# Performance work log

Measured on AMD Instinct MI355X. Metric: run time of the kernel, lower is better.

Reference implementation:

```python
import jax, jax.numpy as jnp
import numpy as np
from jax import lax

L, H, C, V, BLK = 6, 12, 768, 50257, 1024
B, T = 4, 1024
HD = C // H
EPS = 1e-5


def _norm(key, shape, scale=0.02):
    return jax.random.normal(key, shape, dtype=jnp.float32) * scale


def setup_inputs() -> dict:
    key = jax.random.key(0)
    ks = jax.random.split(key, 16)
    idx = jax.random.randint(ks[0], (B, T), 0, V)
    inp = {
        "idx": idx,
        "wte": _norm(ks[1], (V, C)),
        "wpe": _norm(ks[2], (BLK, C)),
        "ln1_s": jnp.ones((L, C)),
        "ln1_b": jnp.zeros((L, C)),
        "qkv_w": _norm(ks[3], (L, C, 3 * C)),
        "qkv_b": jnp.zeros((L, 3 * C)),
        "proj_w": _norm(ks[4], (L, C, C)),
        "proj_b": jnp.zeros((L, C)),
        "ln2_s": jnp.ones((L, C)),
        "ln2_b": jnp.zeros((L, C)),
        "fc_w": _norm(ks[5], (L, C, 4 * C)),
        "fc_b": jnp.zeros((L, 4 * C)),
        "fcp_w": _norm(ks[6], (L, 4 * C, C)),
        "fcp_b": jnp.zeros((L, C)),
        "lnf_s": jnp.ones((C,)),
        "lnf_b": jnp.zeros((C,)),
    }
    return inp


def layer_norm(x, s, b):
    mu = jnp.mean(x, axis=-1, keepdims=True)
    var = jnp.mean(jnp.square(x - mu), axis=-1, keepdims=True)
    return (x - mu) * lax.rsqrt(var + EPS) * s + b


def block(x, p):
    ln1_s, ln1_b, qkv_w, qkv_b, proj_w, proj_b, ln2_s, ln2_b, fc_w, fc_b, fcp_w, fcp_b = p
    Bx, Tx, Cx = x.shape
    h = layer_norm(x, ln1_s, ln1_b)
    qkv = h @ qkv_w + qkv_b  # [B,T,3C]
    q, k, v = jnp.split(qkv, 3, axis=-1)
    q = q.reshape(Bx, Tx, H, HD).swapaxes(1, 2)  # [B,H,T,hd]
    k = k.reshape(Bx, Tx, H, HD).swapaxes(1, 2)
    v = v.reshape(Bx, Tx, H, HD).swapaxes(1, 2)
    attn = jnp.einsum("bhqd,bhkd->bhqk", q, k) / jnp.sqrt(jnp.float32(HD))
    mask = jnp.tril(jnp.ones((Tx, Tx), dtype=bool))
    attn = jnp.where(mask, attn, -jnp.inf)
    attn = jax.nn.softmax(attn, axis=-1)
    y = jnp.einsum("bhqk,bhkd->bhqd", attn, v)
    y = y.swapaxes(1, 2).reshape(Bx, Tx, Cx)
    x = x + (y @ proj_w + proj_b)
    h = layer_norm(x, ln2_s, ln2_b)
    h = jax.nn.gelu(h @ fc_w + fc_b, approximate=True)
    x = x + (h @ fcp_w + fcp_b)
    return x


def reference(idx, wte, wpe, ln1_s, ln1_b, qkv_w, qkv_b, proj_w, proj_b,
              ln2_s, ln2_b, fc_w, fc_b, fcp_w, fcp_b, lnf_s, lnf_b):
    Tx = idx.shape[1]
    x = wte[idx] + wpe[:Tx][None]  # [B,T,C]
    params = (ln1_s, ln1_b, qkv_w, qkv_b, proj_w, proj_b,
              ln2_s, ln2_b, fc_w, fc_b, fcp_w, fcp_b)
    def step(carry, p):
        return block(carry, p), None
    x, _ = lax.scan(step, x, params)
    x = layer_norm(x, lnf_s, lnf_b)
    logits = x @ wte.T  # tied embedding attend
    return logits
```

## Files before the change

kernel.cpp:

```cpp
#include <hip/hip_runtime.h>
#include <math.h>

#define LNUM 6
#define HNUM 12
#define CDIM 768
#define VDIM 50257
#define BDIM 4
#define TDIM 1024
#define NTOK 4096

typedef __bf16 bf16;
typedef __bf16 bf16x8 __attribute__((ext_vector_type(8)));
typedef float  floatx4 __attribute__((ext_vector_type(4)));
typedef unsigned int u32;

__device__ inline void gload16(const bf16* gsrc, bf16* lds) {
  __builtin_amdgcn_global_load_lds(
      (const __attribute__((address_space(1))) u32*)gsrc,
      (__attribute__((address_space(3))) u32*)lds, 16, 0, 0);
}

__global__ void k_cvt_bf16(const float* __restrict__ in, bf16* __restrict__ out, long n) {
  long i = ((long)blockIdx.x * blockDim.x + threadIdx.x) * 4;
  long stride = (long)gridDim.x * blockDim.x * 4;
  for (; i < n; i += stride) {
    float4 v = *reinterpret_cast<const float4*>(in + i);
    bf16 b0 = (bf16)v.x, b1 = (bf16)v.y, b2 = (bf16)v.z, b3 = (bf16)v.w;
    ushort4 pk;
    pk.x = __builtin_bit_cast(unsigned short, b0);
    pk.y = __builtin_bit_cast(unsigned short, b1);
    pk.z = __builtin_bit_cast(unsigned short, b2);
    pk.w = __builtin_bit_cast(unsigned short, b3);
    *reinterpret_cast<ushort4*>(out + i) = pk;
  }
}

#define TILES_QKV  1728
#define TILES_PROJ 576
#define TILES_FC   2304
#define TILES_FCP  2304
#define TILES_LAYER (TILES_QKV + TILES_PROJ + TILES_FC + TILES_FCP)

__global__ __launch_bounds__(256) void k_trans_all(
    const float* __restrict__ qkv_w, const float* __restrict__ proj_w,
    const float* __restrict__ fc_w, const float* __restrict__ fcp_w,
    bf16* __restrict__ wq, bf16* __restrict__ wp,
    bf16* __restrict__ wf, bf16* __restrict__ wfp) {
  __shared__ float tile[32][33];
  int bid = blockIdx.x;
  int layer = bid / TILES_LAYER, r = bid % TILES_LAYER;
  const float* src; bf16* dst; int K, N, tx, ty;
  if (r < TILES_QKV) {
    src = qkv_w + (size_t)layer * CDIM * 3 * CDIM; dst = wq + (size_t)layer * CDIM * 3 * CDIM;
    K = CDIM; N = 3 * CDIM; tx = r % 72; ty = r / 72;
  } else if (r < TILES_QKV + TILES_PROJ) {
    r -= TILES_QKV;
    src = proj_w + (size_t)layer * CDIM * CDIM; dst = wp + (size_t)layer * CDIM * CDIM;
    K = CDIM; N = CDIM; tx = r % 24; ty = r / 24;
  } else if (r < TILES_QKV + TILES_PROJ + TILES_FC) {
    r -= TILES_QKV + TILES_PROJ;
    src = fc_w + (size_t)layer * CDIM * 4 * CDIM; dst = wf + (size_t)layer * CDIM * 4 * CDIM;
    K = CDIM; N = 4 * CDIM; tx = r % 96; ty = r / 96;
  } else {
    r -= TILES_QKV + TILES_PROJ + TILES_FC;
    src = fcp_w + (size_t)layer * 4 * CDIM * CDIM; dst = wfp + (size_t)layer * 4 * CDIM * CDIM;
    K = 4 * CDIM; N = CDIM; tx = r % 24; ty = r / 24;
  }
  int n0 = tx * 32, k0 = ty * 32;
  int nx = threadIdx.x & 31, tyy = threadIdx.x >> 5;
  #pragma unroll
  for (int p = 0; p < 4; ++p) {
    int k = tyy + p * 8;
    tile[k][nx] = src[(size_t)(k0 + k) * N + n0 + nx];
  }
  __syncthreads();
  #pragma unroll
  for (int p = 0; p < 4; ++p) {
    int n = tyy + p * 8;
    dst[(size_t)(n0 + n) * K + k0 + nx] = (bf16)tile[nx][n];
  }
}

__global__ void k_embed(const int* __restrict__ idx, const float* __restrict__ wte,
                        const float* __restrict__ wpe, float* __restrict__ x) {
  int tok = blockIdx.x;
  int t = tok & (TDIM - 1);
  int id = idx[tok];
  const float* a = wte + (size_t)id * CDIM;
  const float* p = wpe + (size_t)t * CDIM;
  float* o = x + (size_t)tok * CDIM;
  for (int c = threadIdx.x; c < CDIM; c += 256) o[c] = a[c] + p[c];
}

__global__ __launch_bounds__(256) void k_layernorm(const float* __restrict__ x,
    const float* __restrict__ sc, const float* __restrict__ bi, bf16* __restrict__ out) {
  __shared__ float red[8];
  int row = blockIdx.x;
  const float* xr = x + (size_t)row * CDIM;
  int t = threadIdx.x;
  float v0 = xr[t], v1 = xr[t + 256], v2 = xr[t + 512];
  float s = v0 + v1 + v2;
  #pragma unroll
  for (int o = 32; o > 0; o >>= 1) s += __shfl_down(s, o);
  if ((t & 63) == 0) red[t >> 6] = s;
  __syncthreads();
  float mean = (red[0] + red[1] + red[2] + red[3]) * (1.0f / CDIM);
  float d0 = v0 - mean, d1 = v1 - mean, d2 = v2 - mean;
  float q = d0 * d0 + d1 * d1 + d2 * d2;
  #pragma unroll
  for (int o = 32; o > 0; o >>= 1) q += __shfl_down(q, o);
  if ((t & 63) == 0) red[4 + (t >> 6)] = q;
  __syncthreads();
  float var = (red[4] + red[5] + red[6] + red[7]) * (1.0f / CDIM);
  float rs = rsqrtf(var + 1e-5f);
  bf16* orow = out + (size_t)row * CDIM;
  orow[t]       = (bf16)(d0 * rs * sc[t]       + bi[t]);
  orow[t + 256] = (bf16)(d1 * rs * sc[t + 256] + bi[t + 256]);
  orow[t + 512] = (bf16)(d2 * rs * sc[t + 512] + bi[t + 512]);
}

__device__ inline float gelu_f(float x) {
  float x3 = x * x * x;
  return 0.5f * x * (1.0f + tanhf(0.7978845608028654f * (x + 0.044715f * x3)));
}

template<int EPI>
__global__ __launch_bounds__(512, 1) void k_gemm8(
    const bf16* __restrict__ A, const bf16* __restrict__ Bt,
    const float* __restrict__ bias,
    float* __restrict__ Cf, bf16* __restrict__ Cb,
    int N, int K) {
  __shared__ __align__(16) bf16 lds[2][4][8192];
  const int nwg = gridDim.x;
  const int id = blockIdx.x;
  const int swz = (id & 7) * (nwg >> 3) + (id >> 3);
  const int m0 = (swz & 15) * 256;
  const int n0 = (swz >> 4) * 256;
  const int tid = threadIdx.x, lane = tid & 63, wave = tid >> 6;
  const int wr = wave >> 2, wc = wave & 3;
  const int g = lane >> 4, r16 = lane & 15;
  const int numK = K >> 6;
  const int wsl = wave * 512;

  const int srow = wave * 16 + (lane >> 2);
  const int scol = ((lane & 3) ^ ((lane >> 3) & 3)) * 8;
  const bf16* at  = A  + (size_t)(m0 + srow) * K + scol;
  const bf16* at1 = A  + (size_t)(m0 + srow + 128) * K + scol;
  const bf16* bt  = Bt + (size_t)(n0 + srow) * K + scol;
  const bf16* bt1 = Bt + (size_t)(n0 + srow + 128) * K + scol;
  const int sw = (g ^ ((r16 >> 1) & 3)) * 8;
  const int a_off = (wr * 128 + r16) * 32 + sw;
  const int b_off = (wc * 64 + r16) * 32 + sw;

  floatx4 acc[8][4] = {};

#define G2(sA, sB, dst) do { gload16((sA), (dst)); gload16((sB), (dst) + 4096); } while (0)

  G2(bt,      bt1,      &lds[0][0][wsl]);
  G2(at,      at1,      &lds[0][1][wsl]);
  G2(bt + 32, bt1 + 32, &lds[0][2][wsl]);
  G2(at + 32, at1 + 32, &lds[0][3][wsl]);
  G2(bt + 64, bt1 + 64, &lds[1][0][wsl]);
  G2(at + 64, at1 + 64, &lds[1][1][wsl]);
  G2(bt + 96, bt1 + 96, &lds[1][2][wsl]);
  asm volatile("s_waitcnt vmcnt(6)" ::: "memory");
  __builtin_amdgcn_s_barrier();

  for (int t = 0; t < numK; ++t) {
    const int p = t & 1, pn = p ^ 1;
    bf16x8 af[4], bfr[4];

    #pragma unroll
    for (int j = 0; j < 4; ++j) bfr[j] = *(const bf16x8*)&lds[p][0][b_off + j * 512];
    #pragma unroll
    for (int i = 0; i < 4; ++i) af[i] = *(const bf16x8*)&lds[p][1][a_off + i * 512];
    if (t + 1 < numK) G2(at + 96, at1 + 96, &lds[pn][3][wsl]);
    __builtin_amdgcn_s_barrier();
    asm volatile("s_waitcnt lgkmcnt(0)" ::: "memory");
    __builtin_amdgcn_s_setprio(1);
    #pragma unroll
    for (int i = 0; i < 4; ++i)
      #pragma unroll
      for (int j = 0; j < 4; ++j)
        acc[i][j] = __builtin_amdgcn_mfma_f32_16x16x32_bf16(af[i], bfr[j], acc[i][j], 0, 0, 0);
    __builtin_amdgcn_s_setprio(0);
    __builtin_amdgcn_s_barrier();

    #pragma unroll
    for (int i = 0; i < 4; ++i) af[i] = *(const bf16x8*)&lds[p][1][a_off + (i + 4) * 512];
    if (t + 2 < numK) G2(bt + 128, bt1 + 128, &lds[p][0][wsl]);
    __builtin_amdgcn_s_barrier();
    asm volatile("s_waitcnt lgkmcnt(0)" ::: "memory");
    __builtin_amdgcn_s_setprio(1);
    #pragma unroll
    for (int i = 0; i < 4; ++i)
      #pragma unroll
      for (int j = 0; j < 4; ++j)
        acc[i + 4][j] = __builtin_amdgcn_mfma_f32_16x16x32_bf16(af[i], bfr[j], acc[i + 4][j], 0, 0, 0);
    __builtin_amdgcn_s_setprio(0);
    __builtin_amdgcn_s_barrier();

    #pragma unroll
    for (int j = 0; j < 4; ++j) bfr[j] = *(const bf16x8*)&lds[p][2][b_off + j * 512];
    #pragma unroll
    for (int i = 0; i < 4; ++i) af[i] = *(const bf16x8*)&lds[p][3][a_off + i * 512];
    if (t + 2 < numK) G2(at + 128, at1 + 128, &lds[p][1][wsl]);
    __builtin_amdgcn_s_barrier();
    asm volatile("s_waitcnt lgkmcnt(0)" ::: "memory");
    __builtin_amdgcn_s_setprio(1);
    #pragma unroll
    for (int i = 0; i < 4; ++i)
      #pragma unroll
      for (int j = 0; j < 4; ++j)
        acc[i][j] = __builtin_amdgcn_mfma_f32_16x16x32_bf16(af[i], bfr[j], acc[i][j], 0, 0, 0);
    __builtin_amdgcn_s_setprio(0);
    __builtin_amdgcn_s_barrier();

    #pragma unroll
    for (int i = 0; i < 4; ++i) af[i] = *(const bf16x8*)&lds[p][3][a_off + (i + 4) * 512];
    if (t + 2 < numK) G2(bt + 160, bt1 + 160, &lds[p][2][wsl]);
    __builtin_amdgcn_s_barrier();
    asm volatile("s_waitcnt lgkmcnt(0)" ::: "memory");
    __builtin_amdgcn_s_setprio(1);
    #pragma unroll
    for (int i = 0; i < 4; ++i)
      #pragma unroll
      for (int j = 0; j < 4; ++j)
        acc[i + 4][j] = __builtin_amdgcn_mfma_f32_16x16x32_bf16(af[i], bfr[j], acc[i + 4][j], 0, 0, 0);
    __builtin_amdgcn_s_setprio(0);
    if (t + 2 < numK) { asm volatile("s_waitcnt vmcnt(6)" ::: "memory"); }
    else              { asm volatile("s_waitcnt vmcnt(0)" ::: "memory"); }
    __builtin_amdgcn_s_barrier();

    at += 64; at1 += 64; bt += 64; bt1 += 64;
  }
#undef G2

  if (EPI == 0) {
    float* sb = reinterpret_cast<float*>(&lds[0][0][0]) + wave * 1088;
    const int seg = lane & 15, rq = lane >> 4;
    const int mrow_base = m0 + wr * 128;
    const int ncol_base = n0 + wc * 64;
    #pragma unroll
    for (int mf = 0; mf < 8; ++mf) {
      #pragma unroll
      for (int nf = 0; nf < 4; ++nf) {
        #pragma unroll
        for (int q = 0; q < 4; ++q)
          sb[(g * 4 + q) * 68 + nf * 16 + r16] = acc[mf][nf][q];
      }
      #pragma unroll
      for (int pz = 0; pz < 4; ++pz) {
        int row = rq + pz * 4;
        floatx4 v = *reinterpret_cast<const floatx4*>(&sb[row * 68 + seg * 4]);
        int m = mrow_base + mf * 16 + row;
        int n = ncol_base + seg * 4;
        if (n + 4 <= N) {
          __builtin_memcpy(&Cf[(size_t)m * N + n], &v, 16);
        } else {
          #pragma unroll
          for (int e = 0; e < 4; ++e)
            if (n + e < N) Cf[(size_t)m * N + n + e] = v[e];
        }
      }
    }
  } else {
    bf16* sb = &lds[0][0][0] + wave * 1152;
    const int rr_rd = lane & 15, seg = lane >> 4;
    const int nb = n0 + wc * 64 + r16;
    float bv[4];
    #pragma unroll
    for (int j = 0; j < 4; ++j) bv[j] = bias[nb + j * 16];
    #pragma unroll
    for (int mf = 0; mf < 8; ++mf) {
      #pragma unroll
      for (int j = 0; j < 4; ++j) {
        #pragma unroll
        for (int q = 0; q < 4; ++q) {
          float v = acc[mf][j][q] + bv[j];
          if (EPI == 3) v = gelu_f(v);
          sb[(g * 4 + q) * 72 + j * 16 + r16] = (bf16)v;
        }
      }
      bf16x8 o0 = *(const bf16x8*)&sb[rr_rd * 72 + seg * 16];
      bf16x8 o1 = *(const bf16x8*)&sb[rr_rd * 72 + seg * 16 + 8];
      size_t orow = (size_t)(m0 + wr * 128 + mf * 16 + rr_rd) * N + (n0 + wc * 64 + seg * 16);
      *(bf16x8*)&Cb[orow] = o0;
      *(bf16x8*)&Cb[orow + 8] = o1;
    }
  }
}

template<int TBM, int MI, int NI, int EPI>
__global__ __launch_bounds__(256) void k_gemm(
    const bf16* __restrict__ A, const bf16* __restrict__ Bt,
    const float* __restrict__ bias, const float* __restrict__ resid,
    float* __restrict__ Cf, bf16* __restrict__ Cb,
    int M, int N, int K) {
  constexpr int BN = 128;
  constexpr int WGN = BN / (NI * 16);
  constexpr int AI = TBM / 32;
  constexpr int BI = BN / 32;
  __shared__ __align__(16) bf16 As[TBM * 64];
  __shared__ __align__(16) bf16 Bs[BN * 64];
  const int m0 = blockIdx.x * TBM, n0 = blockIdx.y * BN;
  const int tid = threadIdx.x;
  const int lane = tid & 63, wave = tid >> 6;
  const int wr = wave / WGN, wc = wave % WGN;
  const int l8 = lane >> 3, s8 = lane & 7;
  const int g = lane >> 4, r16 = lane & 15;

  floatx4 acc[MI][NI] = {};

  const bf16* a_src = A + (size_t)(m0 + l8) * K + s8 * 8;
  const bf16* b_src = Bt + (size_t)(n0 + l8) * K + s8 * 8;

  for (int k0 = 0; k0 < K; k0 += 64) {
    #pragma unroll
    for (int t = 0; t < AI; ++t) {
      int row0 = wave * (TBM / 4) + t * 8;
      gload16(a_src + (size_t)row0 * K + k0, &As[row0 * 64]);
    }
    #pragma unroll
    for (int t = 0; t < BI; ++t) {
      int row0 = wave * 32 + t * 8;
      gload16(b_src + (size_t)row0 * K + k0, &Bs[row0 * 64]);
    }
    __syncthreads();
    #pragma unroll
    for (int kk = 0; kk < 2; ++kk) {
      bf16x8 af[MI], bfr[NI];
      #pragma unroll
      for (int i = 0; i < MI; ++i)
        af[i] = *reinterpret_cast<const bf16x8*>(&As[(wr * MI * 16 + i * 16 + r16) * 64 + g * 8 + kk * 32]);
      #pragma unroll
      for (int j = 0; j < NI; ++j)
        bfr[j] = *reinterpret_cast<const bf16x8*>(&Bs[(wc * NI * 16 + j * 16 + r16) * 64 + g * 8 + kk * 32]);
      #pragma unroll
      for (int i = 0; i < MI; ++i) {
        #pragma unroll
        for (int j = 0; j < NI; ++j)
          acc[i][j] = __builtin_amdgcn_mfma_f32_16x16x32_bf16(af[i], bfr[j], acc[i][j], 0, 0, 0);
      }
    }
    __syncthreads();
  }

  int mb = m0 + wr * MI * 16 + g * 4;
  int nb = n0 + wc * NI * 16 + r16;
  #pragma unroll
  for (int j = 0; j < NI; ++j) {
    int n = nb + j * 16;
    if (n >= N) continue;
    float bv = (EPI >= 2) ? bias[n] : 0.0f;
    #pragma unroll
    for (int i = 0; i < MI; ++i) {
      #pragma unroll
      for (int q = 0; q < 4; ++q) {
        int m = mb + i * 16 + q;
        float v = acc[i][j][q] + bv;
        size_t o = (size_t)m * N + n;
        if (EPI == 2)      Cf[o] = v + resid[o];
        else if (EPI == 3) Cb[o] = (bf16)gelu_f(v);
        else if (EPI == 4) Cb[o] = (bf16)v;
        else               Cf[o] = v;
      }
    }
  }
}

__global__ __launch_bounds__(256) void k_vtrans(const bf16* __restrict__ qkv, bf16* __restrict__ vt) {
  __shared__ bf16 tile[64][72];
  int bh = blockIdx.x, t0 = blockIdx.y * 64;
  int b = bh / HNUM, h = bh % HNUM;
  int tid = threadIdx.x;
  int r8 = tid >> 3, s8 = tid & 7;
  #pragma unroll
  for (int p = 0; p < 2; ++p) {
    int row = p * 32 + r8;
    uint4 v = *reinterpret_cast<const uint4*>(
        qkv + (size_t)(b * TDIM + t0 + row) * (3 * CDIM) + 2 * CDIM + h * 64 + s8 * 8);
    *reinterpret_cast<uint4*>(&tile[row][s8 * 8]) = v;
  }
  __syncthreads();
  int d = tid >> 2, q4 = tid & 3;
  #pragma unroll
  for (int half = 0; half < 2; ++half) {
    int t = q4 * 16 + half * 8;
    bf16x8 o;
    #pragma unroll
    for (int u = 0; u < 8; ++u) o[u] = tile[t + u][d];
    *reinterpret_cast<bf16x8*>(vt + (size_t)bh * (64 * TDIM) + (size_t)d * TDIM + t0 + t) = o;
  }
}

__global__ __launch_bounds__(256) void k_attn(const bf16* __restrict__ qkv,
                                              const bf16* __restrict__ vt,
                                              bf16* __restrict__ y) {
  __shared__ __align__(16) bf16 Ks[64 * 64];
  __shared__ __align__(16) bf16 Vs[64 * 64];
  __shared__ __align__(16) bf16 Ps[64 * 64];
  const int bh = blockIdx.x, qt = blockIdx.y;
  const int b = bh / HNUM, h = bh % HNUM;
  const int tid = threadIdx.x, lane = tid & 63, wave = tid >> 6;
  const int g = lane >> 4, r16 = lane & 15;
  const int w16 = wave * 16;
  const int r8 = tid >> 3, s8 = tid & 7;

  bf16x8 qf[2];
  {
    const bf16* qsrc = qkv + (size_t)(b * TDIM + qt * 64 + w16 + r16) * (3 * CDIM) + h * 64 + g * 8;
    qf[0] = *reinterpret_cast<const bf16x8*>(qsrc);
    qf[1] = *reinterpret_cast<const bf16x8*>(qsrc + 32);
  }

  float m_r[4], l_r[4];
  floatx4 yacc[4] = {};
  #pragma unroll
  for (int q = 0; q < 4; ++q) { m_r[q] = -1e30f; l_r[q] = 0.f; }

  for (int kt = 0; kt <= qt; ++kt) {
    __syncthreads();
    #pragma unroll
    for (int p = 0; p < 2; ++p) {
      int row = p * 32 + r8;
      uint4 kv = *reinterpret_cast<const uint4*>(
          qkv + (size_t)(b * TDIM + kt * 64 + row) * (3 * CDIM) + CDIM + h * 64 + s8 * 8);
      *reinterpret_cast<uint4*>(&Ks[row * 64 + ((s8 ^ (row & 7)) * 8)]) = kv;
      uint4 vv = *reinterpret_cast<const uint4*>(
          vt + (size_t)bh * (64 * TDIM) + (size_t)row * TDIM + kt * 64 + s8 * 8);
      *reinterpret_cast<uint4*>(&Vs[row * 64 + ((s8 ^ (row & 7)) * 8)]) = vv;
    }
    __syncthreads();

    floatx4 sa[4] = {};
    #pragma unroll
    for (int c = 0; c < 2; ++c) {
      bf16x8 kf[4];
      #pragma unroll
      for (int j = 0; j < 4; ++j) {
        int krow = j * 16 + r16;
        kf[j] = *reinterpret_cast<const bf16x8*>(&Ks[krow * 64 + (((g + 4 * c) ^ (krow & 7)) * 8)]);
      }
      #pragma unroll
      for (int j = 0; j < 4; ++j)
        sa[j] = __builtin_amdgcn_mfma_f32_16x16x32_bf16(qf[c], kf[j], sa[j], 0, 0, 0);
    }

    const bool diag = (kt == qt);
    float p_v[4][4];
    #pragma unroll
    for (int q = 0; q < 4; ++q) {
      int qrow = w16 + g * 4 + q;
      float mx = -1e30f;
      #pragma unroll
      for (int j = 0; j < 4; ++j) {
        float s = sa[j][q] * 0.125f;
        if (diag && (r16 + j * 16) > qrow) s = -1e30f;
        p_v[j][q] = s;
        mx = fmaxf(mx, s);
      }
      #pragma unroll
      for (int o = 1; o < 16; o <<= 1) mx = fmaxf(mx, __shfl_xor(mx, o));
      float mnew = fmaxf(m_r[q], mx);
      float ps = 0.f;
      #pragma unroll
      for (int j = 0; j < 4; ++j) {
        float p = __expf(p_v[j][q] - mnew);
        p_v[j][q] = p;
        ps += p;
      }
      #pragma unroll
      for (int o = 1; o < 16; o <<= 1) ps += __shfl_xor(ps, o);
      float alpha = __expf(m_r[q] - mnew);
      m_r[q] = mnew;
      l_r[q] = l_r[q] * alpha + ps;
      #pragma unroll
      for (int j = 0; j < 4; ++j) yacc[j][q] *= alpha;
      #pragma unroll
      for (int j = 0; j < 4; ++j) {
        int col = r16 + j * 16;
        Ps[qrow * 64 + (col ^ ((qrow & 7) << 3))] = (bf16)p_v[j][q];
      }
    }

    #pragma unroll
    for (int ks = 0; ks < 2; ++ks) {
      int prow = w16 + r16;
      bf16x8 pa = *reinterpret_cast<const bf16x8*>(&Ps[prow * 64 + (((g + 4 * ks) ^ (prow & 7)) * 8)]);
      #pragma unroll
      for (int j = 0; j < 4; ++j) {
        int vrow = j * 16 + r16;
        bf16x8 vb = *reinterpret_cast<const bf16x8*>(&Vs[vrow * 64 + (((g + 4 * ks) ^ (vrow & 7)) * 8)]);
        yacc[j] = __builtin_amdgcn_mfma_f32_16x16x32_bf16(pa, vb, yacc[j], 0, 0, 0);
      }
    }
  }

  #pragma unroll
  for (int q = 0; q < 4; ++q) {
    float inv = 1.0f / l_r[q];
    int tok = b * TDIM + qt * 64 + w16 + g * 4 + q;
    #pragma unroll
    for (int j = 0; j < 4; ++j)
      y[(size_t)tok * CDIM + h * 64 + r16 + j * 16] = (bf16)(yacc[j][q] * inv);
  }
}

extern "C" void kernel_launch(void* const* d_in, const int* in_sizes, int n_in,
                              void* d_out, int out_size, void* d_ws, size_t ws_size,
                              hipStream_t stream) {
  (void)in_sizes; (void)n_in; (void)out_size;
  const int*   idx    = (const int*)  d_in[0];
  const float* wte    = (const float*)d_in[1];
  const float* wpe    = (const float*)d_in[2];
  const float* ln1_s  = (const float*)d_in[3];
  const float* ln1_b  = (const float*)d_in[4];
  const float* qkv_w  = (const float*)d_in[5];
  const float* qkv_b  = (const float*)d_in[6];
  const float* proj_w = (const float*)d_in[7];
  const float* proj_b = (const float*)d_in[8];
  const float* ln2_s  = (const float*)d_in[9];
  const float* ln2_b  = (const float*)d_in[10];
  const float* fc_w   = (const float*)d_in[11];
  const float* fc_b   = (const float*)d_in[12];
  const float* fcp_w  = (const float*)d_in[13];
  const float* fcp_b  = (const float*)d_in[14];
  const float* lnf_s  = (const float*)d_in[15];
  const float* lnf_b  = (const float*)d_in[16];
  float* logits = (float*)d_out;

  char* base = (char*)d_ws;
  size_t off = 0;
  auto alloc = [&](size_t bytes) -> void* {
    void* p = base + off;
    off += (bytes + 255) & ~(size_t)255;
    return p;
  };
  bf16*  wte_bf  = (bf16*) alloc((size_t)VDIM * CDIM * 2);
  bf16*  wq_all  = (bf16*) alloc((size_t)LNUM * 3 * CDIM * CDIM * 2);
  bf16*  wp_all  = (bf16*) alloc((size_t)LNUM * CDIM * CDIM * 2);
  bf16*  wf_all  = (bf16*) alloc((size_t)LNUM * 4 * CDIM * CDIM * 2);
  bf16*  wfp_all = (bf16*) alloc((size_t)LNUM * 4 * CDIM * CDIM * 2);
  float* x       = (float*)alloc((size_t)NTOK * CDIM * 4);
  bf16*  hb      = (bf16*) alloc((size_t)NTOK * CDIM * 2);
  bf16*  qkv_bf  = (bf16*) alloc((size_t)NTOK * 3 * CDIM * 2);
  bf16*  vt      = (bf16*) alloc((size_t)BDIM * HNUM * 64 * TDIM * 2);
  bf16*  yb      = (bf16*) alloc((size_t)NTOK * CDIM * 2);
  bf16*  gb      = (bf16*) alloc((size_t)NTOK * 4 * CDIM * 2);
  if (off > ws_size) return;

  k_cvt_bf16<<<4096, 256, 0, stream>>>(wte, wte_bf, (long)VDIM * CDIM);
  k_trans_all<<<LNUM * TILES_LAYER, 256, 0, stream>>>(qkv_w, proj_w, fc_w, fcp_w,
                                                      wq_all, wp_all, wf_all, wfp_all);
  k_embed<<<NTOK, 256, 0, stream>>>(idx, wte, wpe, x);

  for (int l = 0; l < LNUM; ++l) {
    const bf16* wq  = wq_all  + (size_t)l * 3 * CDIM * CDIM;
    const bf16* wp  = wp_all  + (size_t)l * CDIM * CDIM;
    const bf16* wf  = wf_all  + (size_t)l * 4 * CDIM * CDIM;
    const bf16* wfp = wfp_all + (size_t)l * 4 * CDIM * CDIM;

    k_layernorm<<<NTOK, 256, 0, stream>>>(x, ln1_s + l*CDIM, ln1_b + l*CDIM, hb);
    k_gemm8<4><<<16 * 9, 512, 0, stream>>>(hb, wq, qkv_b + (size_t)l*3*CDIM, nullptr, qkv_bf, 3*CDIM, CDIM);
    k_vtrans<<<dim3(BDIM*HNUM, TDIM/64), 256, 0, stream>>>(qkv_bf, vt);
    k_attn<<<dim3(BDIM*HNUM, TDIM/64), 256, 0, stream>>>(qkv_bf, vt, yb);
    k_gemm<64,4,2,2><<<dim3(NTOK/64, 6), 256, 0, stream>>>(yb, wp, proj_b + (size_t)l*CDIM, x, x, nullptr, NTOK, CDIM, CDIM);
    k_layernorm<<<NTOK, 256, 0, stream>>>(x, ln2_s + l*CDIM, ln2_b + l*CDIM, hb);
    k_gemm8<3><<<16 * 12, 512, 0, stream>>>(hb, wf, fc_b + (size_t)l*4*CDIM, nullptr, gb, 4*CDIM, CDIM);
    k_gemm<64,4,2,2><<<dim3(NTOK/64, 6), 256, 0, stream>>>(gb, wfp, fcp_b + (size_t)l*CDIM, x, x, nullptr, NTOK, CDIM, 4*CDIM);
  }

  k_layernorm<<<NTOK, 256, 0, stream>>>(x, lnf_s, lnf_b, hb);
  int ntile = (VDIM + 255) / 256;
  k_gemm8<0><<<16 * ntile, 512, 0, stream>>>(hb, wte_bf, nullptr, logits, nullptr, VDIM, CDIM);
}
```

Before: 1.839 ms.

## Template k_gemm8 on M tile size and halve K-step per pipeline iteration

Makes the 8-wave GEMM kernel templated on M tile height (128 or 256) and shrinks each pipeline iteration from K=64 to K=32 with a two-stage LDS buffer. The QKV and FC GEMMs switch to 128-row tiles, doubling workgroup count (288 and 384 blocks) so more CUs are busy on these small-N problems. The logits GEMM keeps 256-row tiles but also uses the new shorter K step. Shared memory per block drops, at the cost of more barriers per unit of work and less reuse per loaded B tile.

```diff
diff --git a/kernel.cpp b/kernel.cpp
--- a/kernel.cpp
+++ b/kernel.cpp
@@ -124,22 +124,27 @@
   return 0.5f * x * (1.0f + tanhf(0.7978845608028654f * (x + 0.044715f * x3)));
 }
 
-template<int EPI>
+template<int TBM, int EPI>
 __global__ __launch_bounds__(512, 1) void k_gemm8(
     const bf16* __restrict__ A, const bf16* __restrict__ Bt,
     const float* __restrict__ bias,
     float* __restrict__ Cf, bf16* __restrict__ Cb,
     int N, int K) {
-  __shared__ __align__(16) bf16 lds[2][4][8192];
+  constexpr int MI = TBM / 32;
+  constexpr int MH = MI / 2;
+  constexpr int MTILES = 4096 / TBM;
+  __shared__ __align__(16) bf16 smem[2 * 8192 + 2 * TBM * 32];
+  bf16* Bs = smem;
+  bf16* As = smem + 2 * 8192;
   const int nwg = gridDim.x;
   const int id = blockIdx.x;
   const int swz = (id & 7) * (nwg >> 3) + (id >> 3);
-  const int m0 = (swz & 15) * 256;
-  const int n0 = (swz >> 4) * 256;
+  const int m0 = (swz % MTILES) * TBM;
+  const int n0 = (swz / MTILES) * 256;
   const int tid = threadIdx.x, lane = tid & 63, wave = tid >> 6;
   const int wr = wave >> 2, wc = wave & 3;
   const int g = lane >> 4, r16 = lane & 15;
-  const int numK = K >> 6;
+  const int numK = K >> 5;
   const int wsl = wave * 512;
 
   const int srow = wave * 16 + (lane >> 2);
@@ -149,37 +154,36 @@
   const bf16* bt  = Bt + (size_t)(n0 + srow) * K + scol;
   const bf16* bt1 = Bt + (size_t)(n0 + srow + 128) * K + scol;
   const int sw = (g ^ ((r16 >> 1) & 3)) * 8;
-  const int a_off = (wr * 128 + r16) * 32 + sw;
+  const int a_off = (wr * (TBM / 2) + r16) * 32 + sw;
   const int b_off = (wc * 64 + r16) * 32 + sw;
 
-  floatx4 acc[8][4] = {};
-
-#define G2(sA, sB, dst) do { gload16((sA), (dst)); gload16((sB), (dst) + 4096); } while (0)
-
-  G2(bt,      bt1,      &lds[0][0][wsl]);
-  G2(at,      at1,      &lds[0][1][wsl]);
-  G2(bt + 32, bt1 + 32, &lds[0][2][wsl]);
-  G2(at + 32, at1 + 32, &lds[0][3][wsl]);
-  G2(bt + 64, bt1 + 64, &lds[1][0][wsl]);
-  G2(at + 64, at1 + 64, &lds[1][1][wsl]);
-  G2(bt + 96, bt1 + 96, &lds[1][2][wsl]);
-  asm volatile("s_waitcnt vmcnt(6)" ::: "memory");
+  floatx4 acc[MI][4] = {};
+
+#define STB(s0, s1, pb) do { gload16((s0), Bs + (pb) * 8192 + wsl); \
+                             gload16((s1), Bs + (pb) * 8192 + wsl + 4096); } while (0)
+#define STA(s0, s1, pb) do { gload16((s0), As + (pb) * TBM * 32 + wsl); \
+                             if constexpr (TBM == 256) gload16((s1), As + (pb) * TBM * 32 + wsl + 4096); } while (0)
+
+  STB(bt, bt1, 0);
+  STA(at, at1, 0);
+  STB(bt + 32, bt1 + 32, 1);
+  asm volatile("s_waitcnt vmcnt(2)" ::: "memory");
   __builtin_amdgcn_s_barrier();
 
   for (int t = 0; t < numK; ++t) {
     const int p = t & 1, pn = p ^ 1;
-    bf16x8 af[4], bfr[4];
-
-    #pragma unroll
-    for (int j = 0; j < 4; ++j) bfr[j] = *(const bf16x8*)&lds[p][0][b_off + j * 512];
-    #pragma unroll
-    for (int i = 0; i < 4; ++i) af[i] = *(const bf16x8*)&lds[p][1][a_off + i * 512];
-    if (t + 1 < numK) G2(at + 96, at1 + 96, &lds[pn][3][wsl]);
+    bf16x8 af[MH], bfr[4];
+
+    #pragma unroll
+    for (int j = 0; j < 4; ++j) bfr[j] = *(const bf16x8*)&Bs[p * 8192 + b_off + j * 512];
+    #pragma unroll
+    for (int i = 0; i < MH; ++i) af[i] = *(const bf16x8*)&As[p * TBM * 32 + a_off + i * 512];
+    if (t + 1 < numK) STA(at + 32, at1 + 32, pn);
     __builtin_amdgcn_s_barrier();
     asm volatile("s_waitcnt lgkmcnt(0)" ::: "memory");
     __builtin_amdgcn_s_setprio(1);
     #pragma unroll
-    for (int i = 0; i < 4; ++i)
+    for (int i = 0; i < MH; ++i)
       #pragma unroll
       for (int j = 0; j < 4; ++j)
         acc[i][j] = __builtin_amdgcn_mfma_f32_16x16x32_bf16(af[i], bfr[j], acc[i][j], 0, 0, 0);
@@ -187,62 +191,33 @@
     __builtin_amdgcn_s_barrier();
 
     #pragma unroll
-    for (int i = 0; i < 4; ++i) af[i] = *(const bf16x8*)&lds[p][1][a_off + (i + 4) * 512];
-    if (t + 2 < numK) G2(bt + 128, bt1 + 128, &lds[p][0][wsl]);
+    for (int i = 0; i < MH; ++i) af[i] = *(const bf16x8*)&As[p * TBM * 32 + a_off + (i + MH) * 512];
+    if (t + 2 < numK) STB(bt + 64, bt1 + 64, p);
     __builtin_amdgcn_s_barrier();
     asm volatile("s_waitcnt lgkmcnt(0)" ::: "memory");
     __builtin_amdgcn_s_setprio(1);
     #pragma unroll
-    for (int i = 0; i < 4; ++i)
+    for (int i = 0; i < MH; ++i)
       #pragma unroll
       for (int j = 0; j < 4; ++j)
-        acc[i + 4][j] = __builtin_amdgcn_mfma_f32_16x16x32_bf16(af[i], bfr[j], acc[i + 4][j], 0, 0, 0);
+        acc[i + MH][j] = __builtin_amdgcn_mfma_f32_16x16x32_bf16(af[i], bfr[j], acc[i + MH][j], 0, 0, 0);
     __builtin_amdgcn_s_setprio(0);
-    __builtin_amdgcn_s_barrier();
-
-    #pragma unroll
-    for (int j = 0; j < 4; ++j) bfr[j] = *(const bf16x8*)&lds[p][2][b_off + j * 512];
-    #pragma unroll
-    for (int i = 0; i < 4; ++i) af[i] = *(const bf16x8*)&lds[p][3][a_off + i * 512];
-    if (t + 2 < numK) G2(at + 128, at1 + 128, &lds[p][1][wsl]);
-    __builtin_amdgcn_s_barrier();
-    asm volatile("s_waitcnt lgkmcnt(0)" ::: "memory");
-    __builtin_amdgcn_s_setprio(1);
-    #pragma unroll
-    for (int i = 0; i < 4; ++i)
-      #pragma unroll
-      for (int j = 0; j < 4; ++j)
-        acc[i][j] = __builtin_amdgcn_mfma_f32_16x16x32_bf16(af[i], bfr[j], acc[i][j], 0, 0, 0);
-    __builtin_amdgcn_s_setprio(0);
-    __builtin_amdgcn_s_barrier();
-
-    #pragma unroll
-    for (int i = 0; i < 4; ++i) af[i] = *(const bf16x8*)&lds[p][3][a_off + (i + 4) * 512];
-    if (t + 2 < numK) G2(bt + 160, bt1 + 160, &lds[p][2][wsl]);
-    __builtin_amdgcn_s_barrier();
-    asm volatile("s_waitcnt lgkmcnt(0)" ::: "memory");
-    __builtin_amdgcn_s_setprio(1);
-    #pragma unroll
-    for (int i = 0; i < 4; ++i)
-      #pragma unroll
-      for (int j = 0; j < 4; ++j)
-        acc[i + 4][j] = __builtin_amdgcn_mfma_f32_16x16x32_bf16(af[i], bfr[j], acc[i + 4][j], 0, 0, 0);
-    __builtin_amdgcn_s_setprio(0);
-    if (t + 2 < numK) { asm volatile("s_waitcnt vmcnt(6)" ::: "memory"); }
+    if (t + 2 < numK) { asm volatile("s_waitcnt vmcnt(2)" ::: "memory"); }
     else              { asm volatile("s_waitcnt vmcnt(0)" ::: "memory"); }
     __builtin_amdgcn_s_barrier();
 
-    at += 64; at1 += 64; bt += 64; bt1 += 64;
-  }
-#undef G2
+    at += 32; at1 += 32; bt += 32; bt1 += 32;
+  }
+#undef STB
+#undef STA
 
   if (EPI == 0) {
-    float* sb = reinterpret_cast<float*>(&lds[0][0][0]) + wave * 1088;
+    float* sb = reinterpret_cast<float*>(smem) + wave * 1088;
     const int seg = lane & 15, rq = lane >> 4;
-    const int mrow_base = m0 + wr * 128;
+    const int mrow_base = m0 + wr * (TBM / 2);
     const int ncol_base = n0 + wc * 64;
     #pragma unroll
-    for (int mf = 0; mf < 8; ++mf) {
+    for (int mf = 0; mf < MI; ++mf) {
       #pragma unroll
       for (int nf = 0; nf < 4; ++nf) {
         #pragma unroll
@@ -265,14 +240,14 @@
       }
     }
   } else {
-    bf16* sb = &lds[0][0][0] + wave * 1152;
+    bf16* sb = smem + wave * 1152;
     const int rr_rd = lane & 15, seg = lane >> 4;
     const int nb = n0 + wc * 64 + r16;
     float bv[4];
     #pragma unroll
     for (int j = 0; j < 4; ++j) bv[j] = bias[nb + j * 16];
     #pragma unroll
-    for (int mf = 0; mf < 8; ++mf) {
+    for (int mf = 0; mf < MI; ++mf) {
       #pragma unroll
       for (int j = 0; j < 4; ++j) {
         #pragma unroll
@@ -284,7 +259,7 @@
       }
       bf16x8 o0 = *(const bf16x8*)&sb[rr_rd * 72 + seg * 16];
       bf16x8 o1 = *(const bf16x8*)&sb[rr_rd * 72 + seg * 16 + 8];
-      size_t orow = (size_t)(m0 + wr * 128 + mf * 16 + rr_rd) * N + (n0 + wc * 64 + seg * 16);
+      size_t orow = (size_t)(m0 + wr * (TBM / 2) + mf * 16 + rr_rd) * N + (n0 + wc * 64 + seg * 16);
       *(bf16x8*)&Cb[orow] = o0;
       *(bf16x8*)&Cb[orow + 8] = o1;
     }
@@ -562,16 +537,16 @@
     const bf16* wfp = wfp_all + (size_t)l * 4 * CDIM * CDIM;
 
     k_layernorm<<<NTOK, 256, 0, stream>>>(x, ln1_s + l*CDIM, ln1_b + l*CDIM, hb);
-    k_gemm8<4><<<16 * 9, 512, 0, stream>>>(hb, wq, qkv_b + (size_t)l*3*CDIM, nullptr, qkv_bf, 3*CDIM, CDIM);
+    k_gemm8<128,4><<<32 * 9, 512, 0, stream>>>(hb, wq, qkv_b + (size_t)l*3*CDIM, nullptr, qkv_bf, 3*CDIM, CDIM);
     k_vtrans<<<dim3(BDIM*HNUM, TDIM/64), 256, 0, stream>>>(qkv_bf, vt);
     k_attn<<<dim3(BDIM*HNUM, TDIM/64), 256, 0, stream>>>(qkv_bf, vt, yb);
     k_gemm<64,4,2,2><<<dim3(NTOK/64, 6), 256, 0, stream>>>(yb, wp, proj_b + (size_t)l*CDIM, x, x, nullptr, NTOK, CDIM, CDIM);
     k_layernorm<<<NTOK, 256, 0, stream>>>(x, ln2_s + l*CDIM, ln2_b + l*CDIM, hb);
-    k_gemm8<3><<<16 * 12, 512, 0, stream>>>(hb, wf, fc_b + (size_t)l*4*CDIM, nullptr, gb, 4*CDIM, CDIM);
+    k_gemm8<128,3><<<32 * 12, 512, 0, stream>>>(hb, wf, fc_b + (size_t)l*4*CDIM, nullptr, gb, 4*CDIM, CDIM);
     k_gemm<64,4,2,2><<<dim3(NTOK/64, 6), 256, 0, stream>>>(gb, wfp, fcp_b + (size_t)l*CDIM, x, x, nullptr, NTOK, CDIM, 4*CDIM);
   }
 
   k_layernorm<<<NTOK, 256, 0, stream>>>(x, lnf_s, lnf_b, hb);
   int ntile = (VDIM + 255) / 256;
-  k_gemm8<0><<<16 * ntile, 512, 0, stream>>>(hb, wte_bf, nullptr, logits, nullptr, VDIM, CDIM);
-}
+  k_gemm8<256,0><<<16 * ntile, 512, 0, stream>>>(hb, wte_bf, nullptr, logits, nullptr, VDIM, CDIM);
+}
```

Measured after the change: 1.779 ms. 1.03x faster.
